# Optimization experiments

Measured on AMD Instinct MI355X. Metric: run time of the kernel, lower is better.

Reference implementation:

```python
import jax, jax.numpy as jnp
import numpy as np

INPUT_DIM = 1024
NUM_CLASSES = 1024
NUM_EXPERTS = 8
TOP_K = 2
HIDDEN = 128  # hard-coded in Expert


def setup_inputs() -> dict:
    key = jax.random.key(0)
    ks = jax.random.split(key, 7)
    s = 0.02
    return {
        "x": jax.random.normal(ks[0], (16384, INPUT_DIM), dtype=jnp.float32),
        "gate_w": jax.random.normal(ks[1], (INPUT_DIM, NUM_EXPERTS), dtype=jnp.float32) * s,
        "gate_b": jnp.zeros((NUM_EXPERTS,), dtype=jnp.float32),
        "w1": jax.random.normal(ks[2], (NUM_EXPERTS, INPUT_DIM, HIDDEN), dtype=jnp.float32) * s,
        "b1": jnp.zeros((NUM_EXPERTS, HIDDEN), dtype=jnp.float32),
        "w2": jax.random.normal(ks[3], (NUM_EXPERTS, HIDDEN, NUM_CLASSES), dtype=jnp.float32) * s,
        "b2": jnp.zeros((NUM_EXPERTS, NUM_CLASSES), dtype=jnp.float32),
    }


def reference(x, gate_w, gate_b, w1, b1, w2, b2):
    B = x.shape[0]
    # gating: softmax over experts, then top-k
    scores = jax.nn.softmax(x @ gate_w + gate_b, axis=1)          # [B, E]
    top_vals, top_idx = jax.lax.top_k(scores, TOP_K)              # [B, K]
    # dense all-expert compute (E small, fixed), then gather selected outputs
    h = jax.nn.relu(jnp.einsum('bi,eih->ebh', x, w1) + b1[:, None, :])   # [E, B, H]
    y = jnp.einsum('ebh,ehc->ebc', h, w2) + b2[:, None, :]               # [E, B, C]
    y = jnp.transpose(y, (1, 0, 2))                                      # [B, E, C]
    sel = jnp.take_along_axis(y, top_idx[:, :, None], axis=1)            # [B, K, C]
    output = jnp.sum(top_vals[:, :, None] * sel, axis=1)                 # [B, C]
    # gates expanded to [B, K, C] then summed over batch -> [K, C]
    gates_sum = jnp.broadcast_to(jnp.sum(top_vals, axis=0)[:, None], (TOP_K, NUM_CLASSES))
    return (output, gates_sum)
```

## Files before the change

### kernel.cpp

```cpp
#include <hip/hip_runtime.h>

#define B_ROWS  16384
#define IN_DIM  1024
#define NEXP    8
#define HID     128
#define NCLS    1024
#define NPAIR   56
#define MAXW1   520
#define MAXW2   312

#define GATE_BLOCKS (B_ROWS / 8)
#define W1T_BLOCKS  (NEXP * (IN_DIM / 32) * (HID / 32))
#define W2T_BLOCKS  (NEXP * (HID / 32) * (NCLS / 32))

typedef __attribute__((ext_vector_type(8))) short bf16x8;
typedef __attribute__((ext_vector_type(4))) float f32x4;
typedef __attribute__((ext_vector_type(4))) unsigned int u32x4;
typedef __attribute__((ext_vector_type(8))) unsigned short u16x8;

__device__ __forceinline__ unsigned short f2bf(float f) {
  union { float f; unsigned u; } v; v.f = f;
  unsigned r = v.u + 0x7FFFu + ((v.u >> 16) & 1u);
  return (unsigned short)(r >> 16);
}

__device__ __forceinline__ int sw64(int row, int sh) {
  return (row << 6) + ((((sh >> 3) ^ row) & 7) << 3) + (sh & 7);
}
__device__ __forceinline__ int sw256(int row, int sh) {
  return (row << 8) + ((((sh >> 3) ^ row) & 7) << 3) + (sh & 7) + ((sh >> 6) << 6);
}

__global__ __launch_bounds__(256) void prep_kernel(
    const float* __restrict__ x, const float* __restrict__ gw,
    const float* __restrict__ gb, const float* __restrict__ w1,
    const float* __restrict__ w2, unsigned short* __restrict__ xb,
    unsigned short* __restrict__ w1bt, unsigned short* __restrict__ w2bt,
    float2* __restrict__ tval, unsigned char* __restrict__ pairid) {
  __shared__ __attribute__((aligned(16))) unsigned char pmem[NEXP * IN_DIM * 4];
  const int bid = blockIdx.x;
  const int t = threadIdx.x;

  if (bid < GATE_BLOCKS) {
    float (*gws)[IN_DIM] = (float(*)[IN_DIM])pmem;
#pragma unroll
    for (int kk = 0; kk < 4; ++kk) {
      const int k = kk * 256 + t;
      const float4 g0 = *(const float4*)(gw + k * NEXP);
      const float4 g1 = *(const float4*)(gw + k * NEXP + 4);
      gws[0][k] = g0.x; gws[1][k] = g0.y; gws[2][k] = g0.z; gws[3][k] = g0.w;
      gws[4][k] = g1.x; gws[5][k] = g1.y; gws[6][k] = g1.z; gws[7][k] = g1.w;
    }
    __syncthreads();

    const int wave = t >> 6, l = t & 63;
    const int r0 = bid * 8 + wave * 2;

    float4 xv0[4], xv1[4];
#pragma unroll
    for (int j = 0; j < 4; ++j) {
      xv0[j] = *(const float4*)(x + (size_t)r0 * IN_DIM + j * 256 + l * 4);
      xv1[j] = *(const float4*)(x + (size_t)(r0 + 1) * IN_DIM + j * 256 + l * 4);
    }

    if (xb) {
#pragma unroll
      for (int j = 0; j < 4; ++j) {
        uint2 p0, p1;
        p0.x = (unsigned)f2bf(xv0[j].x) | ((unsigned)f2bf(xv0[j].y) << 16);
        p0.y = (unsigned)f2bf(xv0[j].z) | ((unsigned)f2bf(xv0[j].w) << 16);
        p1.x = (unsigned)f2bf(xv1[j].x) | ((unsigned)f2bf(xv1[j].y) << 16);
        p1.y = (unsigned)f2bf(xv1[j].z) | ((unsigned)f2bf(xv1[j].w) << 16);
        *(uint2*)(xb + (size_t)r0 * IN_DIM + j * 256 + l * 4)       = p0;
        *(uint2*)(xb + (size_t)(r0 + 1) * IN_DIM + j * 256 + l * 4) = p1;
      }
    }

    float a0[NEXP], a1[NEXP];
#pragma unroll
    for (int e = 0; e < NEXP; ++e) { a0[e] = 0.f; a1[e] = 0.f; }
#pragma unroll
    for (int e = 0; e < NEXP; ++e) {
#pragma unroll
      for (int j = 0; j < 4; ++j) {
        const float4 g = *(const float4*)&gws[e][j * 256 + l * 4];
        a0[e] = fmaf(xv0[j].x, g.x, a0[e]); a0[e] = fmaf(xv0[j].y, g.y, a0[e]);
        a0[e] = fmaf(xv0[j].z, g.z, a0[e]); a0[e] = fmaf(xv0[j].w, g.w, a0[e]);
        a1[e] = fmaf(xv1[j].x, g.x, a1[e]); a1[e] = fmaf(xv1[j].y, g.y, a1[e]);
        a1[e] = fmaf(xv1[j].z, g.z, a1[e]); a1[e] = fmaf(xv1[j].w, g.w, a1[e]);
      }
    }
#pragma unroll
    for (int e = 0; e < NEXP; ++e) {
#pragma unroll
      for (int off = 32; off > 0; off >>= 1) {
        a0[e] += __shfl_xor(a0[e], off);
        a1[e] += __shfl_xor(a1[e], off);
      }
    }

    if (l == 0) {
#pragma unroll
      for (int rr = 0; rr < 2; ++rr) {
        const float* a = rr ? a1 : a0;
        float lg[NEXP];
#pragma unroll
        for (int e = 0; e < NEXP; ++e) lg[e] = a[e] + gb[e];
        float m = lg[0];
#pragma unroll
        for (int e = 1; e < NEXP; ++e) m = fmaxf(m, lg[e]);
        float p[NEXP], s = 0.f;
#pragma unroll
        for (int e = 0; e < NEXP; ++e) { p[e] = __expf(lg[e] - m); s += p[e]; }
        const float inv = 1.f / s;
        int   i0 = 0;  float v0 = p[0];
#pragma unroll
        for (int e = 1; e < NEXP; ++e) if (p[e] > v0) { v0 = p[e]; i0 = e; }
        int   i1 = -1; float v1 = -1.f;
#pragma unroll
        for (int e = 0; e < NEXP; ++e)
          if (e != i0 && p[e] > v1) { v1 = p[e]; i1 = e; }
        tval[r0 + rr] = make_float2(v0 * inv, v1 * inv);
        pairid[r0 + rr] = (unsigned char)(i0 * 7 + i1 - (i1 > i0 ? 1 : 0));
      }
    }
  } else {
    float (*tile)[33] = (float(*)[33])pmem;
    const float* src; unsigned short* dst;
    int R, C, r0, c0, e;
    if (bid < GATE_BLOCKS + W1T_BLOCKS) {
      const int b1 = bid - GATE_BLOCKS;
      e = b1 >> 7; const int rem = b1 & 127;
      R = IN_DIM; C = HID;
      c0 = (rem & 3) * 32; r0 = (rem >> 2) * 32;
      src = w1; dst = w1bt;
    } else {
      const int b2 = bid - GATE_BLOCKS - W1T_BLOCKS;
      e = b2 >> 7; const int rem = b2 & 127;
      R = HID; C = NCLS;
      c0 = (rem & 31) * 32; r0 = (rem >> 5) * 32;
      src = w2; dst = w2bt;
    }
    src += (size_t)e * R * C;
    dst += (size_t)e * R * C;
    const int tx = t & 31, ty = t >> 5;
#pragma unroll
    for (int i = ty; i < 32; i += 8)
      tile[i][tx] = src[(size_t)(r0 + i) * C + c0 + tx];
    __syncthreads();
#pragma unroll
    for (int i = ty; i < 32; i += 8)
      dst[(size_t)(c0 + i) * R + r0 + tx] = f2bf(tile[tx][i]);
  }
}

__global__ __launch_bounds__(256) void hist_part_kernel(
    const unsigned char* __restrict__ pairid, const float2* __restrict__ tval,
    int* __restrict__ partials, float2* __restrict__ psum) {
  __shared__ int h[64];
  __shared__ float s0a[256], s1a[256];
  const int t = threadIdx.x;
  if (t < 64) h[t] = 0;
  __syncthreads();
  const int row = blockIdx.x * 256 + t;
  const int p  = pairid[row];
  const int ea = p / 7, rem = p % 7;
  const int eb = rem + (rem >= ea ? 1 : 0);
  atomicAdd(&h[p], 1);
  atomicAdd(&h[56 + ea], 1);
  atomicAdd(&h[56 + eb], 1);
  const float2 v = tval[row];
  s0a[t] = v.x; s1a[t] = v.y;
  __syncthreads();
#pragma unroll
  for (int s = 128; s > 0; s >>= 1) {
    if (t < s) { s0a[t] += s0a[t + s]; s1a[t] += s1a[t + s]; }
    __syncthreads();
  }
  if (t < 64) partials[blockIdx.x * 64 + t] = h[t];
  if (t == 0) psum[blockIdx.x] = make_float2(s0a[0], s1a[0]);
}

__global__ void scan_kernel(const int* __restrict__ partials,
                            const float2* __restrict__ psum,
                            int* __restrict__ hist, int* __restrict__ base,
                            int* __restrict__ csr, int* __restrict__ meta,
                            float* __restrict__ out) {
  const int t = threadIdx.x;
  __shared__ float gg[2];
  if (t < 64) {
    int s = 0;
    for (int b = 0; b < B_ROWS / 256; ++b) s += partials[b * 64 + t];
    hist[t] = s;
  }
  if (t == 0) {
    float g0 = 0.f, g1 = 0.f;
    for (int b = 0; b < B_ROWS / 256; ++b) { g0 += psum[b].x; g1 += psum[b].y; }
    gg[0] = g0; gg[1] = g1;
  }
  __syncthreads();
  float* gout = out + (size_t)B_ROWS * NCLS;
  for (int c = t; c < NCLS; c += 64) {
    gout[c]        = gg[0];
    gout[NCLS + c] = gg[1];
  }
  if (t != 0) return;
  int accp = 0, acce = 0;
  for (int p = 0; p < NPAIR; ++p) { base[p] = accp; csr[p] = accp; accp += hist[p]; }
  for (int e = 0; e < NEXP; ++e) {
    base[56 + e] = acce; csr[56 + e] = acce; acce += hist[56 + e];
  }
  int n = 0;
  int* w1 = meta + 2;
  for (int e = 0; e < NEXP; ++e) {
    const int tiles = (hist[56 + e] + 63) >> 6;
    for (int i = 0; i < tiles; ++i) w1[n++] = (e << 16) | i;
  }
  meta[0] = n;
  n = 0;
  int* w2 = meta + 2 + MAXW1;
  for (int p = 0; p < NPAIR; ++p) {
    const int tiles = (hist[p] + 63) >> 6;
    for (int i = 0; i < tiles; ++i) w2[n++] = (p << 16) | i;
  }
  meta[1] = n;
}

__global__ __launch_bounds__(256) void scatter_kernel(
    const unsigned char* __restrict__ pairid, int* __restrict__ csr,
    int* __restrict__ elist, int* __restrict__ plist) {
  __shared__ int h[64], lbase[64];
  const int t = threadIdx.x;
  if (t < 64) h[t] = 0;
  __syncthreads();
  const int row = blockIdx.x * 256 + t;
  const int p  = pairid[row];
  const int ea = p / 7, rem = p % 7;
  const int eb = rem + (rem >= ea ? 1 : 0);
  const int op = atomicAdd(&h[p], 1);
  const int oa = atomicAdd(&h[56 + ea], 1);
  const int ob = atomicAdd(&h[56 + eb], 1);
  __syncthreads();
  if (t < 64) lbase[t] = h[t] ? atomicAdd(&csr[t], h[t]) : 0;
  __syncthreads();
  plist[lbase[p] + op]       = row;
  elist[lbase[56 + ea] + oa] = (row << 1);
  elist[lbase[56 + eb] + ob] = (row << 1) | 1;
}

template <bool XB>
__global__ __launch_bounds__(256) void k1_hidden(
    const float* __restrict__ x, const unsigned short* __restrict__ xb,
    const unsigned short* __restrict__ w1bt, const float* __restrict__ b1,
    const float2* __restrict__ tval, const int* __restrict__ elist,
    const int* __restrict__ hist, const int* __restrict__ base,
    const int* __restrict__ meta, unsigned short* __restrict__ Hg) {
  const int b = blockIdx.x;
  if (b >= meta[0]) return;
  const int item = meta[2 + b];
  const int e = item >> 16, tile = item & 0xffff;
  const int start = tile * 64;
  const int nr = min(64, hist[56 + e] - start);

  __shared__ unsigned short As[64 * 64];
  __shared__ unsigned short Bs[128 * 64];
  __shared__ int rowl[64];

  const int t = threadIdx.x;
  if (t < 64) rowl[t] = elist[base[56 + e] + start + (t < nr ? t : 0)];
  __syncthreads();

  const int wid = t >> 6, l = t & 63;
  const int wr = wid >> 1, wc = wid & 1;
  const int lg = l >> 4,   ln = l & 15;

  f32x4 acc[2][4];
#pragma unroll
  for (int ms = 0; ms < 2; ++ms)
#pragma unroll
    for (int nf = 0; nf < 4; ++nf) acc[ms][nf] = (f32x4){0.f, 0.f, 0.f, 0.f};

  const int ai = t >> 2, aseg = t & 3;
  const float* asrcf = x + (size_t)(rowl[ai] >> 1) * IN_DIM + aseg * 16;
  const unsigned short* asrcb =
      xb + (size_t)(rowl[ai] >> 1) * IN_DIM + aseg * 16;
  const int bn = t >> 1, bhf = t & 1;
  const unsigned short* bsrc =
      w1bt + ((size_t)e * HID + bn) * IN_DIM + bhf * 32;

  if constexpr (XB) {
    u32x4 areg[2], breg[4];
    {
      const u32x4* ap = (const u32x4*)(asrcb);
      areg[0] = ap[0]; areg[1] = ap[1];
      const u32x4* bp = (const u32x4*)(bsrc);
#pragma unroll
      for (int j = 0; j < 4; ++j) breg[j] = bp[j];
    }
    for (int ks = 0; ks < 16; ++ks) {
      *(u32x4*)&As[sw64(ai, aseg * 16)]     = areg[0];
      *(u32x4*)&As[sw64(ai, aseg * 16 + 8)] = areg[1];
#pragma unroll
      for (int j = 0; j < 4; ++j)
        *(u32x4*)&Bs[sw64(bn, bhf * 32 + j * 8)] = breg[j];
      __syncthreads();
      if (ks < 15) {
        const u32x4* ap = (const u32x4*)(asrcb + (ks + 1) * 64);
        areg[0] = ap[0]; areg[1] = ap[1];
        const u32x4* bp = (const u32x4*)(bsrc + (ks + 1) * 64);
#pragma unroll
        for (int j = 0; j < 4; ++j) breg[j] = bp[j];
      }
      bf16x8 af[2][2], bf[4][2];
#pragma unroll
      for (int ms = 0; ms < 2; ++ms)
#pragma unroll
        for (int kh = 0; kh < 2; ++kh)
          af[ms][kh] = *(const bf16x8*)&As[sw64(wr*32 + ms*16 + ln, kh*32 + lg*8)];
#pragma unroll
      for (int nf = 0; nf < 4; ++nf)
#pragma unroll
        for (int kh = 0; kh < 2; ++kh)
          bf[nf][kh] = *(const bf16x8*)&Bs[sw64(wc*64 + nf*16 + ln, kh*32 + lg*8)];
#pragma unroll
      for (int ms = 0; ms < 2; ++ms)
#pragma unroll
        for (int nf = 0; nf < 4; ++nf) {
          acc[ms][nf] = __builtin_amdgcn_mfma_f32_16x16x32_bf16(af[ms][0], bf[nf][0], acc[ms][nf], 0, 0, 0);
          acc[ms][nf] = __builtin_amdgcn_mfma_f32_16x16x32_bf16(af[ms][1], bf[nf][1], acc[ms][nf], 0, 0, 0);
        }
      __syncthreads();
    }
  } else {
    for (int ks = 0; ks < 16; ++ks) {
      {
        const float4 f0 = *(const float4*)(asrcf + ks * 64);
        const float4 f1 = *(const float4*)(asrcf + ks * 64 + 4);
        const float4 f2 = *(const float4*)(asrcf + ks * 64 + 8);
        const float4 f3 = *(const float4*)(asrcf + ks * 64 + 12);
        u16x8 u0, u1;
        u0[0]=f2bf(f0.x); u0[1]=f2bf(f0.y); u0[2]=f2bf(f0.z); u0[3]=f2bf(f0.w);
        u0[4]=f2bf(f1.x); u0[5]=f2bf(f1.y); u0[6]=f2bf(f1.z); u0[7]=f2bf(f1.w);
        u1[0]=f2bf(f2.x); u1[1]=f2bf(f2.y); u1[2]=f2bf(f2.z); u1[3]=f2bf(f2.w);
        u1[4]=f2bf(f3.x); u1[5]=f2bf(f3.y); u1[6]=f2bf(f3.z); u1[7]=f2bf(f3.w);
        *(u16x8*)&As[sw64(ai, aseg * 16)]     = u0;
        *(u16x8*)&As[sw64(ai, aseg * 16 + 8)] = u1;
      }
      {
        const u32x4* bp = (const u32x4*)(bsrc + ks * 64);
#pragma unroll
        for (int j = 0; j < 4; ++j)
          *(u32x4*)&Bs[sw64(bn, bhf * 32 + j * 8)] = bp[j];
      }
      __syncthreads();
      bf16x8 af[2][2], bf[4][2];
#pragma unroll
      for (int ms = 0; ms < 2; ++ms)
#pragma unroll
        for (int kh = 0; kh < 2; ++kh)
          af[ms][kh] = *(const bf16x8*)&As[sw64(wr*32 + ms*16 + ln, kh*32 + lg*8)];
#pragma unroll
      for (int nf = 0; nf < 4; ++nf)
#pragma unroll
        for (int kh = 0; kh < 2; ++kh)
          bf[nf][kh] = *(const bf16x8*)&Bs[sw64(wc*64 + nf*16 + ln, kh*32 + lg*8)];
#pragma unroll
      for (int ms = 0; ms < 2; ++ms)
#pragma unroll
        for (int nf = 0; nf < 4; ++nf) {
          acc[ms][nf] = __builtin_amdgcn_mfma_f32_16x16x32_bf16(af[ms][0], bf[nf][0], acc[ms][nf], 0, 0, 0);
          acc[ms][nf] = __builtin_amdgcn_mfma_f32_16x16x32_bf16(af[ms][1], bf[nf][1], acc[ms][nf], 0, 0, 0);
        }
      __syncthreads();
    }
  }

  float b1c[4];
#pragma unroll
  for (int nf = 0; nf < 4; ++nf) b1c[nf] = b1[e * HID + wc*64 + nf*16 + ln];

#pragma unroll
  for (int ms = 0; ms < 2; ++ms)
#pragma unroll
    for (int r = 0; r < 4; ++r) {
      const int li = wr*32 + ms*16 + lg*4 + r;
      if (li < nr) {
        const int packed = rowl[li];
        const int row = packed >> 1, slot = packed & 1;
        const float2 tv = tval[row];
        const float v = slot ? tv.y : tv.x;
#pragma unroll
        for (int nf = 0; nf < 4; ++nf) {
          const float h = fmaxf(acc[ms][nf][r] + b1c[nf], 0.f) * v;
          Hg[((size_t)row * 2 + slot) * HID + wc*64 + nf*16 + ln] = f2bf(h);
        }
      }
    }
}

__global__ __launch_bounds__(256) void k2_out(
    const unsigned short* __restrict__ Hg, const unsigned short* __restrict__ w2bt,
    const float* __restrict__ b2, const float2* __restrict__ tval,
    const int* __restrict__ plist, const int* __restrict__ hist,
    const int* __restrict__ base, const int* __restrict__ meta,
    float* __restrict__ out) {
  const int b = blockIdx.y;
  if (b >= meta[1]) return;
  const int item = meta[2 + MAXW1 + b];
  const int p = item >> 16, rt = item & 0xffff;
  const int ea = p / 7, rem = p % 7;
  const int eb = rem + (rem >= ea ? 1 : 0);
  const int start = rt * 64;
  const int nr = min(64, hist[p] - start);
  const int c0 = blockIdx.x * 128;

  __shared__ unsigned short Ah[64 * 256];
  __shared__ unsigned short Bs[128 * 64];
  __shared__ int rowl[64];
  __shared__ float2 vals[64];

  const int t = threadIdx.x;
  if (t < 64) {
    const int r = plist[base[p] + start + (t < nr ? t : 0)];
    rowl[t] = r;
    vals[t] = tval[r];
  }
  __syncthreads();

  {
    const int i = t >> 2, q = t & 3;
    const u32x4* src = (const u32x4*)(Hg + (size_t)rowl[i] * 256 + q * 64);
#pragma unroll
    for (int j = 0; j < 8; ++j)
      *(u32x4*)&Ah[sw256(i, q * 64 + j * 8)] = src[j];
  }

  const int wid = t >> 6, l = t & 63;
  const int wr = wid >> 1, wc = wid & 1;
  const int lg = l >> 4,   ln = l & 15;

  f32x4 acc[2][4];
#pragma unroll
  for (int ms = 0; ms < 2; ++ms)
#pragma unroll
    for (int nf = 0; nf < 4; ++nf) acc[ms][nf] = (f32x4){0.f, 0.f, 0.f, 0.f};

  const int bn = t >> 1, bhf = t & 1;
  u32x4 breg[4];
  {
    const u32x4* bp = (const u32x4*)(
        w2bt + ((size_t)ea * NCLS + c0 + bn) * HID + bhf * 32);
#pragma unroll
    for (int j = 0; j < 4; ++j) breg[j] = bp[j];
  }
#pragma unroll
  for (int ks = 0; ks < 4; ++ks) {
#pragma unroll
    for (int j = 0; j < 4; ++j)
      *(u32x4*)&Bs[sw64(bn, bhf * 32 + j * 8)] = breg[j];
    __syncthreads();
    if (ks < 3) {
      const int exn = (ks + 1 < 2) ? ea : eb;
      const int hbn = ((ks + 1) & 1) * 64;
      const u32x4* bp = (const u32x4*)(
          w2bt + ((size_t)exn * NCLS + c0 + bn) * HID + hbn + bhf * 32);
#pragma unroll
      for (int j = 0; j < 4; ++j) breg[j] = bp[j];
    }
    bf16x8 af[2][2], bf[4][2];
#pragma unroll
    for (int ms = 0; ms < 2; ++ms)
#pragma unroll
      for (int kh = 0; kh < 2; ++kh)
        af[ms][kh] = *(const bf16x8*)&Ah[sw256(wr*32 + ms*16 + ln, ks*64 + kh*32 + lg*8)];
#pragma unroll
    for (int nf = 0; nf < 4; ++nf)
#pragma unroll
      for (int kh = 0; kh < 2; ++kh)
        bf[nf][kh] = *(const bf16x8*)&Bs[sw64(wc*64 + nf*16 + ln, kh*32 + lg*8)];
#pragma unroll
    for (int ms = 0; ms < 2; ++ms)
#pragma unroll
      for (int nf = 0; nf < 4; ++nf) {
        acc[ms][nf] = __builtin_amdgcn_mfma_f32_16x16x32_bf16(af[ms][0], bf[nf][0], acc[ms][nf], 0, 0, 0);
        acc[ms][nf] = __builtin_amdgcn_mfma_f32_16x16x32_bf16(af[ms][1], bf[nf][1], acc[ms][nf], 0, 0, 0);
      }
    __syncthreads();
  }

  float b2a[4], b2b[4];
#pragma unroll
  for (int nf = 0; nf < 4; ++nf) {
    const int c = c0 + wc*64 + nf*16 + ln;
    b2a[nf] = b2[ea * NCLS + c];
    b2b[nf] = b2[eb * NCLS + c];
  }
#pragma unroll
  for (int ms = 0; ms < 2; ++ms)
#pragma unroll
    for (int r = 0; r < 4; ++r) {
      const int li = wr*32 + ms*16 + lg*4 + r;
      if (li < nr) {
        const int row = rowl[li];
        const float2 v = vals[li];
#pragma unroll
        for (int nf = 0; nf < 4; ++nf) {
          const int c = c0 + wc*64 + nf*16 + ln;
          out[(size_t)row * NCLS + c] = acc[ms][nf][r] + v.x * b2a[nf] + v.y * b2b[nf];
        }
      }
    }
}

extern "C" void kernel_launch(void* const* d_in, const int* in_sizes, int n_in,
                              void* d_out, int out_size, void* d_ws, size_t ws_size,
                              hipStream_t stream) {
  const float* x   = (const float*)d_in[0];
  const float* gw  = (const float*)d_in[1];
  const float* gb  = (const float*)d_in[2];
  const float* w1  = (const float*)d_in[3];
  const float* b1  = (const float*)d_in[4];
  const float* w2  = (const float*)d_in[5];
  const float* b2  = (const float*)d_in[6];
  float* out = (float*)d_out;

  char* ws = (char*)d_ws;
  int*            hist     = (int*)(ws);
  int*            base     = (int*)(ws + 256);
  int*            csr      = (int*)(ws + 512);
  int*            meta     = (int*)(ws + 768);
  int*            partials = (int*)(ws + 4352);
  float2*         psum     = (float2*)(ws + 20736);
  unsigned char*  pairid   = (unsigned char*)(ws + 21248);
  float2*         tval     = (float2*)(ws + 37632);
  int*            elist    = (int*)(ws + 168704);
  int*            plist    = (int*)(ws + 299776);
  unsigned short* w1bt     = (unsigned short*)(ws + 365312);
  unsigned short* w2bt     = (unsigned short*)(ws + 2462464);
  unsigned short* Hg       = (unsigned short*)(ws + 4559616);
  const bool use_xb = (ws_size >= (size_t)46502656);
  unsigned short* xb = use_xb ? (unsigned short*)(ws + 12948224) : nullptr;

  prep_kernel<<<GATE_BLOCKS + W1T_BLOCKS + W2T_BLOCKS, 256, 0, stream>>>(
      x, gw, gb, w1, w2, xb, w1bt, w2bt, tval, pairid);
  hist_part_kernel<<<B_ROWS / 256, 256, 0, stream>>>(pairid, tval, partials, psum);
  scan_kernel<<<1, 64, 0, stream>>>(partials, psum, hist, base, csr, meta, out);
  scatter_kernel<<<B_ROWS / 256, 256, 0, stream>>>(pairid, csr, elist, plist);

  if (use_xb)
    k1_hidden<true><<<MAXW1, 256, 0, stream>>>(x, xb, w1bt, b1, tval, elist,
                                               hist, base, meta, Hg);
  else
    k1_hidden<false><<<MAXW1, 256, 0, stream>>>(x, xb, w1bt, b1, tval, elist,
                                                hist, base, meta, Hg);
  k2_out<<<dim3(NCLS / 128, MAXW2), 256, 0, stream>>>(Hg, w2bt, b2, tval, plist,
                                                      hist, base, meta, out);
}
```

Baseline: 118.0 us.

## Fuse routing kernels into cooperative launch and widen k2 column tile

Merges the histogram, scan and scatter kernels into one cooperative kernel that uses grid-wide syncs, removing two kernel launches and their gaps. The gate-sum reduction now uses a wavefront shuffle instead of a serial loop. Separately, k2_out doubles its column tile from 128 to 256, so A-tile loads are shared across more output columns, at the cost of more LDS and accumulator registers per block and half as many blocks. Grid sync relies on all 64 blocks being co-resident, and the larger tile may lower occupancy.

Result: slower. 162.4 us (+37.6%).

```diff
diff --git a/kernel.cpp b/kernel.cpp
--- a/kernel.cpp
+++ b/kernel.cpp
@@ -1,4 +1,7 @@
 #include <hip/hip_runtime.h>
+#include <hip/hip_cooperative_groups.h>
+
+namespace cg = cooperative_groups;
 
 #define B_ROWS  16384
 #define IN_DIM  1024
@@ -154,93 +157,90 @@
   }
 }
 
-__global__ __launch_bounds__(256) void hist_part_kernel(
+__global__ __launch_bounds__(256) void sort_kernel(
     const unsigned char* __restrict__ pairid, const float2* __restrict__ tval,
-    int* __restrict__ partials, float2* __restrict__ psum) {
-  __shared__ int h[64];
+    int* __restrict__ partials, float2* __restrict__ psum,
+    int* __restrict__ hist, int* __restrict__ base, int* __restrict__ csr,
+    int* __restrict__ meta, int* __restrict__ elist, int* __restrict__ plist,
+    float* __restrict__ out) {
+  __shared__ int h[64], lbase[64];
   __shared__ float s0a[256], s1a[256];
   const int t = threadIdx.x;
+  const int bid = blockIdx.x;
+
   if (t < 64) h[t] = 0;
   __syncthreads();
-  const int row = blockIdx.x * 256 + t;
-  const int p  = pairid[row];
-  const int ea = p / 7, rem = p % 7;
-  const int eb = rem + (rem >= ea ? 1 : 0);
-  atomicAdd(&h[p], 1);
-  atomicAdd(&h[56 + ea], 1);
-  atomicAdd(&h[56 + eb], 1);
-  const float2 v = tval[row];
-  s0a[t] = v.x; s1a[t] = v.y;
-  __syncthreads();
-#pragma unroll
-  for (int s = 128; s > 0; s >>= 1) {
-    if (t < s) { s0a[t] += s0a[t + s]; s1a[t] += s1a[t + s]; }
-    __syncthreads();
-  }
-  if (t < 64) partials[blockIdx.x * 64 + t] = h[t];
-  if (t == 0) psum[blockIdx.x] = make_float2(s0a[0], s1a[0]);
-}
-
-__global__ void scan_kernel(const int* __restrict__ partials,
-                            const float2* __restrict__ psum,
-                            int* __restrict__ hist, int* __restrict__ base,
-                            int* __restrict__ csr, int* __restrict__ meta,
-                            float* __restrict__ out) {
-  const int t = threadIdx.x;
-  __shared__ float gg[2];
-  if (t < 64) {
-    int s = 0;
-    for (int b = 0; b < B_ROWS / 256; ++b) s += partials[b * 64 + t];
-    hist[t] = s;
-  }
-  if (t == 0) {
-    float g0 = 0.f, g1 = 0.f;
-    for (int b = 0; b < B_ROWS / 256; ++b) { g0 += psum[b].x; g1 += psum[b].y; }
-    gg[0] = g0; gg[1] = g1;
-  }
-  __syncthreads();
-  float* gout = out + (size_t)B_ROWS * NCLS;
-  for (int c = t; c < NCLS; c += 64) {
-    gout[c]        = gg[0];
-    gout[NCLS + c] = gg[1];
-  }
-  if (t != 0) return;
-  int accp = 0, acce = 0;
-  for (int p = 0; p < NPAIR; ++p) { base[p] = accp; csr[p] = accp; accp += hist[p]; }
-  for (int e = 0; e < NEXP; ++e) {
-    base[56 + e] = acce; csr[56 + e] = acce; acce += hist[56 + e];
-  }
-  int n = 0;
-  int* w1 = meta + 2;
-  for (int e = 0; e < NEXP; ++e) {
-    const int tiles = (hist[56 + e] + 63) >> 6;
-    for (int i = 0; i < tiles; ++i) w1[n++] = (e << 16) | i;
-  }
-  meta[0] = n;
-  n = 0;
-  int* w2 = meta + 2 + MAXW1;
-  for (int p = 0; p < NPAIR; ++p) {
-    const int tiles = (hist[p] + 63) >> 6;
-    for (int i = 0; i < tiles; ++i) w2[n++] = (p << 16) | i;
-  }
-  meta[1] = n;
-}
-
-__global__ __launch_bounds__(256) void scatter_kernel(
-    const unsigned char* __restrict__ pairid, int* __restrict__ csr,
-    int* __restrict__ elist, int* __restrict__ plist) {
-  __shared__ int h[64], lbase[64];
-  const int t = threadIdx.x;
-  if (t < 64) h[t] = 0;
-  __syncthreads();
-  const int row = blockIdx.x * 256 + t;
+  const int row = bid * 256 + t;
   const int p  = pairid[row];
   const int ea = p / 7, rem = p % 7;
   const int eb = rem + (rem >= ea ? 1 : 0);
   const int op = atomicAdd(&h[p], 1);
   const int oa = atomicAdd(&h[56 + ea], 1);
   const int ob = atomicAdd(&h[56 + eb], 1);
+  const float2 v = tval[row];
+  s0a[t] = v.x; s1a[t] = v.y;
   __syncthreads();
+#pragma unroll
+  for (int s = 128; s > 0; s >>= 1) {
+    if (t < s) { s0a[t] += s0a[t + s]; s1a[t] += s1a[t + s]; }
+    __syncthreads();
+  }
+  if (t < 64) partials[bid * 64 + t] = h[t];
+  if (t == 0) psum[bid] = make_float2(s0a[0], s1a[0]);
+
+  __threadfence();
+  cg::this_grid().sync();
+
+  if (bid == 0) {
+    if (t < 64) {
+      int s = 0;
+      for (int b = 0; b < B_ROWS / 256; ++b) s += partials[b * 64 + t];
+      hist[t] = s;
+    }
+    __syncthreads();
+    if (t == 0) {
+      int accp = 0, acce = 0;
+      for (int q = 0; q < NPAIR; ++q) { base[q] = accp; csr[q] = accp; accp += hist[q]; }
+      for (int e = 0; e < NEXP; ++e) {
+        base[56 + e] = acce; csr[56 + e] = acce; acce += hist[56 + e];
+      }
+      int n = 0;
+      int* w1m = meta + 2;
+      for (int e = 0; e < NEXP; ++e) {
+        const int tiles = (hist[56 + e] + 63) >> 6;
+        for (int i = 0; i < tiles; ++i) w1m[n++] = (e << 16) | i;
+      }
+      meta[0] = n;
+      n = 0;
+      int* w2m = meta + 2 + MAXW1;
+      for (int q = 0; q < NPAIR; ++q) {
+        const int tiles = (hist[q] + 63) >> 6;
+        for (int i = 0; i < tiles; ++i) w2m[n++] = (q << 16) | i;
+      }
+      meta[1] = n;
+    }
+  } else if (bid == 1) {
+    __shared__ float gg[2];
+    if (t < 64) {
+      float g0 = psum[t].x, g1 = psum[t].y;
+#pragma unroll
+      for (int off = 32; off > 0; off >>= 1) {
+        g0 += __shfl_xor(g0, off);
+        g1 += __shfl_xor(g1, off);
+      }
+      if (t == 0) { gg[0] = g0; gg[1] = g1; }
+    }
+    __syncthreads();
+    float* gout = out + (size_t)B_ROWS * NCLS;
+    for (int c = t; c < NCLS; c += 256) {
+      gout[c]        = gg[0];
+      gout[NCLS + c] = gg[1];
+    }
+  }
+
+  __threadfence();
+  cg::this_grid().sync();
+
   if (t < 64) lbase[t] = h[t] ? atomicAdd(&csr[t], h[t]) : 0;
   __syncthreads();
   plist[lbase[p] + op]       = row;
@@ -388,11 +388,11 @@
         const int packed = rowl[li];
         const int row = packed >> 1, slot = packed & 1;
         const float2 tv = tval[row];
-        const float v = slot ? tv.y : tv.x;
+        const float vv = slot ? tv.y : tv.x;
 #pragma unroll
         for (int nf = 0; nf < 4; ++nf) {
-          const float h = fmaxf(acc[ms][nf][r] + b1c[nf], 0.f) * v;
-          Hg[((size_t)row * 2 + slot) * HID + wc*64 + nf*16 + ln] = f2bf(h);
+          const float hh = fmaxf(acc[ms][nf][r] + b1c[nf], 0.f) * vv;
+          Hg[((size_t)row * 2 + slot) * HID + wc*64 + nf*16 + ln] = f2bf(hh);
         }
       }
     }
@@ -412,10 +412,10 @@
   const int eb = rem + (rem >= ea ? 1 : 0);
   const int start = rt * 64;
   const int nr = min(64, hist[p] - start);
-  const int c0 = blockIdx.x * 128;
+  const int c0 = blockIdx.x * 256;
 
   __shared__ unsigned short Ah[64 * 256];
-  __shared__ unsigned short Bs[128 * 64];
+  __shared__ unsigned short Bs[256 * 64];
   __shared__ int rowl[64];
   __shared__ float2 vals[64];
 
@@ -439,59 +439,56 @@
   const int wr = wid >> 1, wc = wid & 1;
   const int lg = l >> 4,   ln = l & 15;
 
-  f32x4 acc[2][4];
+  f32x4 acc[2][8];
 #pragma unroll
   for (int ms = 0; ms < 2; ++ms)
 #pragma unroll
-    for (int nf = 0; nf < 4; ++nf) acc[ms][nf] = (f32x4){0.f, 0.f, 0.f, 0.f};
-
-  const int bn = t >> 1, bhf = t & 1;
-  u32x4 breg[4];
+    for (int nf = 0; nf < 8; ++nf) acc[ms][nf] = (f32x4){0.f, 0.f, 0.f, 0.f};
+
+  const int bn = t;
+  u32x4 breg[8];
   {
-    const u32x4* bp = (const u32x4*)(
-        w2bt + ((size_t)ea * NCLS + c0 + bn) * HID + bhf * 32);
-#pragma unroll
-    for (int j = 0; j < 4; ++j) breg[j] = bp[j];
+    const u32x4* bp = (const u32x4*)(w2bt + ((size_t)ea * NCLS + c0 + bn) * HID);
+#pragma unroll
+    for (int j = 0; j < 8; ++j) breg[j] = bp[j];
   }
 #pragma unroll
   for (int ks = 0; ks < 4; ++ks) {
 #pragma unroll
-    for (int j = 0; j < 4; ++j)
-      *(u32x4*)&Bs[sw64(bn, bhf * 32 + j * 8)] = breg[j];
+    for (int j = 0; j < 8; ++j)
+      *(u32x4*)&Bs[sw64(bn, j * 8)] = breg[j];
     __syncthreads();
     if (ks < 3) {
       const int exn = (ks + 1 < 2) ? ea : eb;
       const int hbn = ((ks + 1) & 1) * 64;
       const u32x4* bp = (const u32x4*)(
-          w2bt + ((size_t)exn * NCLS + c0 + bn) * HID + hbn + bhf * 32);
-#pragma unroll
-      for (int j = 0; j < 4; ++j) breg[j] = bp[j];
-    }
-    bf16x8 af[2][2], bf[4][2];
+          w2bt + ((size_t)exn * NCLS + c0 + bn) * HID + hbn);
+#pragma unroll
+      for (int j = 0; j < 8; ++j) breg[j] = bp[j];
+    }
+    bf16x8 af[2][2];
 #pragma unroll
     for (int ms = 0; ms < 2; ++ms)
 #pragma unroll
       for (int kh = 0; kh < 2; ++kh)
         af[ms][kh] = *(const bf16x8*)&Ah[sw256(wr*32 + ms*16 + ln, ks*64 + kh*32 + lg*8)];
 #pragma unroll
-    for (int nf = 0; nf < 4; ++nf)
-#pragma unroll
-      for (int kh = 0; kh < 2; ++kh)
-        bf[nf][kh] = *(const bf16x8*)&Bs[sw64(wc*64 + nf*16 + ln, kh*32 + lg*8)];
-#pragma unroll
-    for (int ms = 0; ms < 2; ++ms)
-#pragma unroll
-      for (int nf = 0; nf < 4; ++nf) {
-        acc[ms][nf] = __builtin_amdgcn_mfma_f32_16x16x32_bf16(af[ms][0], bf[nf][0], acc[ms][nf], 0, 0, 0);
-        acc[ms][nf] = __builtin_amdgcn_mfma_f32_16x16x32_bf16(af[ms][1], bf[nf][1], acc[ms][nf], 0, 0, 0);
-      }
-    __syncthreads();
-  }
-
-  float b2a[4], b2b[4];
-#pragma unroll
-  for (int nf = 0; nf < 4; ++nf) {
-    const int c = c0 + wc*64 + nf*16 + ln;
+    for (int nf = 0; nf < 8; ++nf) {
+      const bf16x8 bf0 = *(const bf16x8*)&Bs[sw64(wc*128 + nf*16 + ln, lg*8)];
+      const bf16x8 bf1 = *(const bf16x8*)&Bs[sw64(wc*128 + nf*16 + ln, 32 + lg*8)];
+#pragma unroll
+      for (int ms = 0; ms < 2; ++ms) {
+        acc[ms][nf] = __builtin_amdgcn_mfma_f32_16x16x32_bf16(af[ms][0], bf0, acc[ms][nf], 0, 0, 0);
+        acc[ms][nf] = __builtin_amdgcn_mfma_f32_16x16x32_bf16(af[ms][1], bf1, acc[ms][nf], 0, 0, 0);
+      }
+    }
+    __syncthreads();
+  }
+
+  float b2a[8], b2b[8];
+#pragma unroll
+  for (int nf = 0; nf < 8; ++nf) {
+    const int c = c0 + wc*128 + nf*16 + ln;
     b2a[nf] = b2[ea * NCLS + c];
     b2b[nf] = b2[eb * NCLS + c];
   }
@@ -504,8 +501,8 @@
         const int row = rowl[li];
         const float2 v = vals[li];
 #pragma unroll
-        for (int nf = 0; nf < 4; ++nf) {
-          const int c = c0 + wc*64 + nf*16 + ln;
+        for (int nf = 0; nf < 8; ++nf) {
+          const int c = c0 + wc*128 + nf*16 + ln;
           out[(size_t)row * NCLS + c] = acc[ms][nf][r] + v.x * b2a[nf] + v.y * b2b[nf];
         }
       }
@@ -543,9 +540,26 @@
 
   prep_kernel<<<GATE_BLOCKS + W1T_BLOCKS + W2T_BLOCKS, 256, 0, stream>>>(
       x, gw, gb, w1, w2, xb, w1bt, w2bt, tval, pairid);
-  hist_part_kernel<<<B_ROWS / 256, 256, 0, stream>>>(pairid, tval, partials, psum);
-  scan_kernel<<<1, 64, 0, stream>>>(partials, psum, hist, base, csr, meta, out);
-  scatter_kernel<<<B_ROWS / 256, 256, 0, stream>>>(pairid, csr, elist, plist);
+
+  {
+    const unsigned char* pairid_a = pairid;
+    const float2* tval_a = tval;
+    int* partials_a = partials;
+    float2* psum_a = psum;
+    int* hist_a = hist;
+    int* base_a = base;
+    int* csr_a = csr;
+    int* meta_a = meta;
+    int* elist_a = elist;
+    int* plist_a = plist;
+    float* out_a = out;
+    void* args[] = {(void*)&pairid_a, (void*)&tval_a, (void*)&partials_a,
+                    (void*)&psum_a,   (void*)&hist_a, (void*)&base_a,
+                    (void*)&csr_a,    (void*)&meta_a, (void*)&elist_a,
+                    (void*)&plist_a,  (void*)&out_a};
+    hipLaunchCooperativeKernel((void*)sort_kernel, dim3(B_ROWS / 256),
+                               dim3(256), args, 0, stream);
+  }
 
   if (use_xb)
     k1_hidden<true><<<MAXW1, 256, 0, stream>>>(x, xb, w1bt, b1, tval, elist,
@@ -553,6 +567,6 @@
   else
     k1_hidden<false><<<MAXW1, 256, 0, stream>>>(x, xb, w1bt, b1, tval, elist,
                                                 hist, base, meta, Hg);
-  k2_out<<<dim3(NCLS / 128, MAXW2), 256, 0, stream>>>(Hg, w2bt, b2, tval, plist,
+  k2_out<<<dim3(NCLS / 256, MAXW2), 256, 0, stream>>>(Hg, w2bt, b2, tval, plist,
                                                       hist, base, meta, out);
 }
```

## Load MFMA operands directly from global memory in k2_out, dropping LDS staging

Applied to the files above, without the earlier changes.

The second-layer kernel no longer stages the gathered hidden rows and expert weight tiles through shared memory. Each lane now loads its bf16 MFMA fragments straight from global memory, with a two-deep register double buffer across the eight K steps, and all __syncthreads in the main loop are gone. Launch bounds now request four blocks per CU. This removes LDS traffic and barriers, but lanes issue uncoalesced 16-byte global loads, and several waves that share the same rows or columns reread them instead of reusing them through LDS.

After: 145.1 us. +23.0%, slower.

```diff
diff --git a/kernel.cpp b/kernel.cpp
--- a/kernel.cpp
+++ b/kernel.cpp
@@ -26,9 +26,6 @@
 
 __device__ __forceinline__ int sw64(int row, int sh) {
   return (row << 6) + ((((sh >> 3) ^ row) & 7) << 3) + (sh & 7);
-}
-__device__ __forceinline__ int sw256(int row, int sh) {
-  return (row << 8) + ((((sh >> 3) ^ row) & 7) << 3) + (sh & 7) + ((sh >> 6) << 6);
 }
 
 __global__ __launch_bounds__(256) void prep_kernel(
@@ -388,17 +385,17 @@
         const int packed = rowl[li];
         const int row = packed >> 1, slot = packed & 1;
         const float2 tv = tval[row];
-        const float v = slot ? tv.y : tv.x;
+        const float vv = slot ? tv.y : tv.x;
 #pragma unroll
         for (int nf = 0; nf < 4; ++nf) {
-          const float h = fmaxf(acc[ms][nf][r] + b1c[nf], 0.f) * v;
-          Hg[((size_t)row * 2 + slot) * HID + wc*64 + nf*16 + ln] = f2bf(h);
+          const float hh = fmaxf(acc[ms][nf][r] + b1c[nf], 0.f) * vv;
+          Hg[((size_t)row * 2 + slot) * HID + wc*64 + nf*16 + ln] = f2bf(hh);
         }
       }
     }
 }
 
-__global__ __launch_bounds__(256) void k2_out(
+__global__ __launch_bounds__(256, 4) void k2_out(
     const unsigned short* __restrict__ Hg, const unsigned short* __restrict__ w2bt,
     const float* __restrict__ b2, const float2* __restrict__ tval,
     const int* __restrict__ plist, const int* __restrict__ hist,
@@ -414,8 +411,6 @@
   const int nr = min(64, hist[p] - start);
   const int c0 = blockIdx.x * 128;
 
-  __shared__ unsigned short Ah[64 * 256];
-  __shared__ unsigned short Bs[128 * 64];
   __shared__ int rowl[64];
   __shared__ float2 vals[64];
 
@@ -427,65 +422,53 @@
   }
   __syncthreads();
 
-  {
-    const int i = t >> 2, q = t & 3;
-    const u32x4* src = (const u32x4*)(Hg + (size_t)rowl[i] * 256 + q * 64);
-#pragma unroll
-    for (int j = 0; j < 8; ++j)
-      *(u32x4*)&Ah[sw256(i, q * 64 + j * 8)] = src[j];
-  }
-
   const int wid = t >> 6, l = t & 63;
   const int wr = wid >> 1, wc = wid & 1;
   const int lg = l >> 4,   ln = l & 15;
 
+  const unsigned short* arow0 = Hg + (size_t)rowl[wr*32 + ln]      * 256 + lg*8;
+  const unsigned short* arow1 = Hg + (size_t)rowl[wr*32 + 16 + ln] * 256 + lg*8;
+  const size_t eaOff = (size_t)ea * NCLS * HID;
+  const size_t ebOff = (size_t)eb * NCLS * HID;
+  const unsigned short* bcol0 = w2bt + (size_t)(c0 + wc*64 +  0 + ln) * HID + lg*8;
+  const unsigned short* bcol1 = w2bt + (size_t)(c0 + wc*64 + 16 + ln) * HID + lg*8;
+  const unsigned short* bcol2 = w2bt + (size_t)(c0 + wc*64 + 32 + ln) * HID + lg*8;
+  const unsigned short* bcol3 = w2bt + (size_t)(c0 + wc*64 + 48 + ln) * HID + lg*8;
+
   f32x4 acc[2][4];
 #pragma unroll
   for (int ms = 0; ms < 2; ++ms)
 #pragma unroll
     for (int nf = 0; nf < 4; ++nf) acc[ms][nf] = (f32x4){0.f, 0.f, 0.f, 0.f};
 
-  const int bn = t >> 1, bhf = t & 1;
-  u32x4 breg[4];
-  {
-    const u32x4* bp = (const u32x4*)(
-        w2bt + ((size_t)ea * NCLS + c0 + bn) * HID + bhf * 32);
-#pragma unroll
-    for (int j = 0; j < 4; ++j) breg[j] = bp[j];
-  }
-#pragma unroll
-  for (int ks = 0; ks < 4; ++ks) {
-#pragma unroll
-    for (int j = 0; j < 4; ++j)
-      *(u32x4*)&Bs[sw64(bn, bhf * 32 + j * 8)] = breg[j];
-    __syncthreads();
-    if (ks < 3) {
-      const int exn = (ks + 1 < 2) ? ea : eb;
-      const int hbn = ((ks + 1) & 1) * 64;
-      const u32x4* bp = (const u32x4*)(
-          w2bt + ((size_t)exn * NCLS + c0 + bn) * HID + hbn + bhf * 32);
-#pragma unroll
-      for (int j = 0; j < 4; ++j) breg[j] = bp[j];
-    }
-    bf16x8 af[2][2], bf[4][2];
-#pragma unroll
-    for (int ms = 0; ms < 2; ++ms)
-#pragma unroll
-      for (int kh = 0; kh < 2; ++kh)
-        af[ms][kh] = *(const bf16x8*)&Ah[sw256(wr*32 + ms*16 + ln, ks*64 + kh*32 + lg*8)];
-#pragma unroll
-    for (int nf = 0; nf < 4; ++nf)
-#pragma unroll
-      for (int kh = 0; kh < 2; ++kh)
-        bf[nf][kh] = *(const bf16x8*)&Bs[sw64(wc*64 + nf*16 + ln, kh*32 + lg*8)];
-#pragma unroll
-    for (int ms = 0; ms < 2; ++ms)
-#pragma unroll
-      for (int nf = 0; nf < 4; ++nf) {
-        acc[ms][nf] = __builtin_amdgcn_mfma_f32_16x16x32_bf16(af[ms][0], bf[nf][0], acc[ms][nf], 0, 0, 0);
-        acc[ms][nf] = __builtin_amdgcn_mfma_f32_16x16x32_bf16(af[ms][1], bf[nf][1], acc[ms][nf], 0, 0, 0);
-      }
-    __syncthreads();
+  bf16x8 afb[2][2], bfb[2][4];
+  afb[0][0] = *(const bf16x8*)(arow0);
+  afb[0][1] = *(const bf16x8*)(arow1);
+  bfb[0][0] = *(const bf16x8*)(bcol0 + eaOff);
+  bfb[0][1] = *(const bf16x8*)(bcol1 + eaOff);
+  bfb[0][2] = *(const bf16x8*)(bcol2 + eaOff);
+  bfb[0][3] = *(const bf16x8*)(bcol3 + eaOff);
+
+#pragma unroll
+  for (int q = 0; q < 8; ++q) {
+    const int cur = q & 1, nxt = cur ^ 1;
+    if (q < 7) {
+      const int qn = q + 1;
+      const size_t eo = (qn < 4) ? eaOff : ebOff;
+      const int ka = qn * 32;
+      const int kb = (qn & 3) * 32;
+      afb[nxt][0] = *(const bf16x8*)(arow0 + ka);
+      afb[nxt][1] = *(const bf16x8*)(arow1 + ka);
+      bfb[nxt][0] = *(const bf16x8*)(bcol0 + eo + kb);
+      bfb[nxt][1] = *(const bf16x8*)(bcol1 + eo + kb);
+      bfb[nxt][2] = *(const bf16x8*)(bcol2 + eo + kb);
+      bfb[nxt][3] = *(const bf16x8*)(bcol3 + eo + kb);
+    }
+#pragma unroll
+    for (int nf = 0; nf < 4; ++nf) {
+      acc[0][nf] = __builtin_amdgcn_mfma_f32_16x16x32_bf16(afb[cur][0], bfb[cur][nf], acc[0][nf], 0, 0, 0);
+      acc[1][nf] = __builtin_amdgcn_mfma_f32_16x16x32_bf16(afb[cur][1], bfb[cur][nf], acc[1][nf], 0, 0, 0);
+    }
   }
 
   float b2a[4], b2b[4];
```
